# Kernel optimization log

Measured on AMD Instinct MI355X. Metric: run time of the kernel, lower is better.

Reference implementation:

```python
import jax, jax.numpy as jnp
import numpy as np
from jax import lax

K = 16        # patch_size / kernel_size
S = 16        # stride
EMB = 768     # embed_dim
CIN = 3


def setup_inputs() -> dict:
    key = jax.random.key(0)
    k1, k2, k3, k4, k5 = jax.random.split(key, 5)
    B, H, W = 64, 384, 384
    pixel_values = jax.random.normal(k1, (B, CIN, H, W), jnp.float32)
    # offset conv: Conv2d(3, 2*K*K, kernel=K, stride=K); small init so offsets stay moderate
    offset_w = jax.random.normal(k2, (2 * K * K, CIN, K, K), jnp.float32) * 0.01
    offset_b = jax.random.normal(k3, (2 * K * K,), jnp.float32) * 0.01
    # deformable projection: DeformConv2d(3, 768, kernel=K, stride=K)
    proj_w = jax.random.normal(k4, (EMB, CIN, K, K), jnp.float32) * 0.02
    proj_b = jax.random.normal(k5, (EMB,), jnp.float32) * 0.02
    return {"pixel_values": pixel_values, "offset_w": offset_w, "offset_b": offset_b,
            "proj_w": proj_w, "proj_b": proj_b}


def _bilinear_gather(img, py, px):
    """img: [B,C,H,W]; py,px: [B,K,K,HO,WO] float sample coords.
    Returns [B,C,K,K,HO,WO] with zero padding outside the image (torchvision semantics)."""
    B, C, H, W = img.shape
    shp = py.shape
    y0 = jnp.floor(py); x0 = jnp.floor(px)
    wy1 = py - y0; wy0 = 1.0 - wy1
    wx1 = px - x0; wx0 = 1.0 - wx1
    imgf = img.reshape(B, C, H * W)

    def corner(yy, xx, w):
        valid = (yy >= 0) & (yy < H) & (xx >= 0) & (xx < W)
        yi = jnp.clip(yy, 0, H - 1).astype(jnp.int32)
        xi = jnp.clip(xx, 0, W - 1).astype(jnp.int32)
        idx = (yi * W + xi).reshape(B, -1)                       # [B, N]
        v = jnp.take_along_axis(imgf, idx[:, None, :], axis=2)   # [B, C, N]
        return v * (jnp.where(valid, w, 0.0)).reshape(B, 1, -1)

    val = (corner(y0, x0, wy0 * wx0) + corner(y0, x0 + 1, wy0 * wx1)
           + corner(y0 + 1, x0, wy1 * wx0) + corner(y0 + 1, x0 + 1, wy1 * wx1))
    return val.reshape((B, C) + shp[1:])


def reference(pixel_values, offset_w, offset_b, proj_w, proj_b):
    B, C, H, W = pixel_values.shape
    HO, WO = H // S, W // S
    # offset conv (dense, stride=patch, VALID padding)
    offset = lax.conv_general_dilated(pixel_values, offset_w, (S, S), 'VALID',
                                      dimension_numbers=('NCHW', 'OIHW', 'NCHW'))
    offset = offset + offset_b[None, :, None, None]              # [B, 2*K*K, HO, WO]
    off = offset.reshape(B, K * K, 2, HO, WO)
    dy = off[:, :, 0].reshape(B, K, K, HO, WO)
    dx = off[:, :, 1].reshape(B, K, K, HO, WO)
    # base sampling grid: p = (ho*S + i + dy, wo*S + j + dx)
    base_y = (jnp.arange(HO, dtype=jnp.float32) * S)[None, None, None, :, None] \
             + jnp.arange(K, dtype=jnp.float32)[None, :, None, None, None]
    base_x = (jnp.arange(WO, dtype=jnp.float32) * S)[None, None, None, None, :] \
             + jnp.arange(K, dtype=jnp.float32)[None, None, :, None, None]
    py = base_y + dy
    px = base_x + dx
    sampled = _bilinear_gather(pixel_values, py, px)             # [B, C, K, K, HO, WO]
    out = jnp.einsum('bcijhw,ocij->bohw', sampled, proj_w) + proj_b[None, :, None, None]
    # flatten(2).transpose(1,2) -> [B, HO*WO, EMB]
    return out.reshape(B, EMB, HO * WO).transpose(0, 2, 1)
```

## Files before the change

kernel.cpp:

```cpp
#include <hip/hip_runtime.h>
#include <stdint.h>

typedef __bf16 bf16x8 __attribute__((ext_vector_type(8)));
typedef float  f32x4  __attribute__((ext_vector_type(4)));

#define HH 384
#define WW 384
#define NPIX (HH*WW)
#define NC 3
#define NPATCH 576
#define EMB 768
#define PLEN 768
#define MLOC 32
#define KSTEPS 24
#define NLOC (64*576)
#define NT1 4
#define NT2 6
#define W1_UNITS (32*KSTEPS*64)
#define W2_UNITS (48*KSTEPS*64)
#define W2_OFF   (W1_UNITS*8)

__device__ __forceinline__ uint16_t f2bf(float f) {
    uint32_t u = __builtin_bit_cast(uint32_t, f);
    u += 0x7FFFu + ((u >> 16) & 1u);
    return (uint16_t)(u >> 16);
}
__device__ __forceinline__ uint32_t pk2(float a, float b) {
    return (uint32_t)f2bf(a) | ((uint32_t)f2bf(b) << 16);
}

__global__ __launch_bounds__(256)
void convert_weights(const float* __restrict__ offw, const float* __restrict__ projw,
                     uint16_t* __restrict__ wz) {
    int u = blockIdx.x * 256 + threadIdx.x;
    const float* src;
    int uu;
    if (u < W1_UNITS) { src = offw; uu = u; }
    else              { src = projw; uu = u - W1_UNITS; }
    int lane = uu & 63;
    int t    = uu >> 6;
    int ks   = t % KSTEPS;
    int nt   = t / KSTEPS;
    int n    = nt * 16 + (lane & 15);
    int k0   = ks * 32 + (lane >> 4) * 8;
    const float4* s4 = (const float4*)(src + (size_t)n * PLEN + k0);
    float4 v0 = s4[0], v1 = s4[1];
    uint4 w;
    w.x = pk2(v0.x, v0.y); w.y = pk2(v0.z, v0.w);
    w.z = pk2(v1.x, v1.y); w.w = pk2(v1.z, v1.w);
    *(uint4*)(wz + (size_t)u * 8) = w;
}

template<bool USE_WS>
__global__ __launch_bounds__(512, 4)
void fused_kernel(const float* __restrict__ pix,
                  const float* __restrict__ offw,
                  const float* __restrict__ offb,
                  const float* __restrict__ projw,
                  const float* __restrict__ projb,
                  const uint16_t* __restrict__ wz,
                  float* __restrict__ out) {
    __shared__ __align__(16) uint16_t As[MLOC][PLEN];

    const int tid  = threadIdx.x;
    const int wv   = tid >> 6;
    const int lane = tid & 63;
    const int lr   = lane & 15;
    const int lg   = lane >> 4;

    int bid = (int)blockIdx.x;
    bid = (bid & 7) * 144 + (bid >> 3);

    const int loc0 = bid * MLOC;
    const int bimg = loc0 / NPATCH;
    const int p0   = loc0 - bimg * NPATCH;
    const float* __restrict__ pb = pix + (size_t)bimg * NC * NPIX;

    #pragma unroll
    for (int uu = 0; uu < 6; ++uu) {
        int unit = tid + uu * 512;
        int loc  = unit / 96;
        int k8   = (unit - loc * 96) * 8;
        int c  = k8 >> 8;
        int i  = (k8 >> 4) & 15;
        int j  = k8 & 15;
        int p  = p0 + loc;
        int ho = p / 24;
        int wo = p - ho * 24;
        const float* g = pb + ((size_t)c * HH + ho * 16 + i) * WW + wo * 16 + j;
        float4 v0 = *(const float4*)g;
        float4 v1 = *(const float4*)(g + 4);
        uint4 w;
        w.x = pk2(v0.x, v0.y); w.y = pk2(v0.z, v0.w);
        w.z = pk2(v1.x, v1.y); w.w = pk2(v1.z, v1.w);
        *(uint4*)&As[loc][k8 ^ ((loc & 7) << 3)] = w;
    }

    const int sw0 = (lr & 7) << 3;

    auto ldb1 = [&](int ntg, int ks) -> bf16x8 {
        if (USE_WS) {
            return *(const bf16x8*)(wz + ((size_t)((ntg * KSTEPS + ks) * 64 + lane)) * 8);
        } else {
            int n = ntg * 16 + lr;
            const float4* s4 = (const float4*)(offw + (size_t)n * PLEN + ks * 32 + lg * 8);
            float4 v0 = s4[0], v1 = s4[1];
            uint4 uq = {pk2(v0.x,v0.y), pk2(v0.z,v0.w), pk2(v1.x,v1.y), pk2(v1.z,v1.w)};
            return __builtin_bit_cast(bf16x8, uq);
        }
    };
    bf16x8 b1a[NT1], b1b[NT1];
    #pragma unroll
    for (int nt = 0; nt < NT1; ++nt) b1a[nt] = ldb1(wv * NT1 + nt, 0);
    __syncthreads();

    f32x4 acc1[2][NT1];
    #pragma unroll
    for (int nt = 0; nt < NT1; ++nt) {
        float bz = offb[(wv * NT1 + nt) * 16 + lr];
        f32x4 z = {bz, bz, bz, bz};
        acc1[0][nt] = z; acc1[1][nt] = z;
    }
    #pragma unroll 1
    for (int ks2 = 0; ks2 < KSTEPS / 2; ++ks2) {
        const int ks0 = ks2 * 2;
        {
            #pragma unroll
            for (int nt = 0; nt < NT1; ++nt) b1b[nt] = ldb1(wv * NT1 + nt, ks0 + 1);
            int ke = (ks0 * 32 + lg * 8) ^ sw0;
            bf16x8 a0 = *(const bf16x8*)&As[lr][ke];
            bf16x8 a1 = *(const bf16x8*)&As[16 + lr][ke];
            __builtin_amdgcn_s_setprio(1);
            #pragma unroll
            for (int nt = 0; nt < NT1; ++nt) {
                acc1[0][nt] = __builtin_amdgcn_mfma_f32_16x16x32_bf16(a0, b1a[nt], acc1[0][nt], 0, 0, 0);
                acc1[1][nt] = __builtin_amdgcn_mfma_f32_16x16x32_bf16(a1, b1a[nt], acc1[1][nt], 0, 0, 0);
            }
            __builtin_amdgcn_s_setprio(0);
        }
        {
            int ksn = (ks0 + 2 < KSTEPS) ? ks0 + 2 : 0;
            #pragma unroll
            for (int nt = 0; nt < NT1; ++nt) b1a[nt] = ldb1(wv * NT1 + nt, ksn);
            int ke = ((ks0 + 1) * 32 + lg * 8) ^ sw0;
            bf16x8 a0 = *(const bf16x8*)&As[lr][ke];
            bf16x8 a1 = *(const bf16x8*)&As[16 + lr][ke];
            __builtin_amdgcn_s_setprio(1);
            #pragma unroll
            for (int nt = 0; nt < NT1; ++nt) {
                acc1[0][nt] = __builtin_amdgcn_mfma_f32_16x16x32_bf16(a0, b1b[nt], acc1[0][nt], 0, 0, 0);
                acc1[1][nt] = __builtin_amdgcn_mfma_f32_16x16x32_bf16(a1, b1b[nt], acc1[1][nt], 0, 0, 0);
            }
            __builtin_amdgcn_s_setprio(0);
        }
    }
    __syncthreads();

    const int even = ((lane & 1) == 0);
    float dyg[2][2][4], dxg[2][2][4];
    #pragma unroll
    for (int nt = 0; nt < NT1; ++nt)
      #pragma unroll
      for (int mt = 0; mt < 2; ++mt)
        #pragma unroll
        for (int r = 0; r < 4; ++r) {
            float v  = acc1[mt][nt][r];
            float pv = __shfl_xor(v, 1);
            if ((nt < 2) == (even != 0)) {
                int s = nt & 1;
                dyg[s][mt][r] = even ? v  : pv;
                dxg[s][mt][r] = even ? pv : v;
            }
        }

    const int ntb  = wv * NT1 + (even ? 0 : 2);
    const int qlow = lr >> 1;
    #pragma unroll
    for (int s = 0; s < 2; ++s) {
        int q  = (ntb + s) * 8 + qlow;
        int qi = q >> 4;
        int qj = q & 15;
        #pragma unroll
        for (int mt = 0; mt < 2; ++mt)
          #pragma unroll
          for (int r = 0; r < 4; ++r) {
            int locl = mt * 16 + lg * 4 + r;
            int p  = p0 + locl;
            int ho = p / 24;
            int wo = p - ho * 24;
            float py = (float)(ho * 16 + qi) + dyg[s][mt][r];
            float px = (float)(wo * 16 + qj) + dxg[s][mt][r];
            float y0f = floorf(py), x0f = floorf(px);
            float wy1 = py - y0f, wy0 = 1.f - wy1;
            float wx1 = px - x0f, wx0 = 1.f - wx1;
            int y0 = (int)y0f, x0 = (int)x0f;
            float s0 = 0.f, s1 = 0.f, s2 = 0.f;
            #pragma unroll
            for (int cy = 0; cy < 2; ++cy) {
                int yy = y0 + cy;
                if ((unsigned)yy < (unsigned)HH) {
                    float wy = cy ? wy1 : wy0;
                    #pragma unroll
                    for (int cx = 0; cx < 2; ++cx) {
                        int xx = x0 + cx;
                        if ((unsigned)xx < (unsigned)WW) {
                            float w = wy * (cx ? wx1 : wx0);
                            const float* cp = pb + yy * WW + xx;
                            s0 += w * cp[0];
                            s1 += w * cp[NPIX];
                            s2 += w * cp[2 * NPIX];
                        }
                    }
                }
            }
            int swl = (locl & 7) << 3;
            As[locl][(      q) ^ swl] = f2bf(s0);
            As[locl][(256 + q) ^ swl] = f2bf(s1);
            As[locl][(512 + q) ^ swl] = f2bf(s2);
          }
    }

    auto ldb2 = [&](int ntg, int ks) -> bf16x8 {
        if (USE_WS) {
            return *(const bf16x8*)(wz + W2_OFF + ((size_t)((ntg * KSTEPS + ks) * 64 + lane)) * 8);
        } else {
            int n = ntg * 16 + lr;
            const float4* s4 = (const float4*)(projw + (size_t)n * PLEN + ks * 32 + lg * 8);
            float4 v0 = s4[0], v1 = s4[1];
            uint4 uq = {pk2(v0.x,v0.y), pk2(v0.z,v0.w), pk2(v1.x,v1.y), pk2(v1.z,v1.w)};
            return __builtin_bit_cast(bf16x8, uq);
        }
    };
    bf16x8 b2a[NT2], b2b[NT2];
    #pragma unroll
    for (int nt = 0; nt < NT2; ++nt) b2a[nt] = ldb2(wv * NT2 + nt, 0);
    __syncthreads();

    f32x4 acc2[2][NT2];
    #pragma unroll
    for (int nt = 0; nt < NT2; ++nt) {
        float bz = projb[(wv * NT2 + nt) * 16 + lr];
        f32x4 z = {bz, bz, bz, bz};
        acc2[0][nt] = z; acc2[1][nt] = z;
    }
    #pragma unroll 1
    for (int ks2 = 0; ks2 < KSTEPS / 2; ++ks2) {
        const int ks0 = ks2 * 2;
        {
            #pragma unroll
            for (int nt = 0; nt < NT2; ++nt) b2b[nt] = ldb2(wv * NT2 + nt, ks0 + 1);
            int ke = (ks0 * 32 + lg * 8) ^ sw0;
            bf16x8 a0 = *(const bf16x8*)&As[lr][ke];
            bf16x8 a1 = *(const bf16x8*)&As[16 + lr][ke];
            __builtin_amdgcn_s_setprio(1);
            #pragma unroll
            for (int nt = 0; nt < NT2; ++nt) {
                acc2[0][nt] = __builtin_amdgcn_mfma_f32_16x16x32_bf16(a0, b2a[nt], acc2[0][nt], 0, 0, 0);
                acc2[1][nt] = __builtin_amdgcn_mfma_f32_16x16x32_bf16(a1, b2a[nt], acc2[1][nt], 0, 0, 0);
            }
            __builtin_amdgcn_s_setprio(0);
        }
        {
            int ksn = (ks0 + 2 < KSTEPS) ? ks0 + 2 : 0;
            #pragma unroll
            for (int nt = 0; nt < NT2; ++nt) b2a[nt] = ldb2(wv * NT2 + nt, ksn);
            int ke = ((ks0 + 1) * 32 + lg * 8) ^ sw0;
            bf16x8 a0 = *(const bf16x8*)&As[lr][ke];
            bf16x8 a1 = *(const bf16x8*)&As[16 + lr][ke];
            __builtin_amdgcn_s_setprio(1);
            #pragma unroll
            for (int nt = 0; nt < NT2; ++nt) {
                acc2[0][nt] = __builtin_amdgcn_mfma_f32_16x16x32_bf16(a0, b2b[nt], acc2[0][nt], 0, 0, 0);
                acc2[1][nt] = __builtin_amdgcn_mfma_f32_16x16x32_bf16(a1, b2b[nt], acc2[1][nt], 0, 0, 0);
            }
            __builtin_amdgcn_s_setprio(0);
        }
    }

    #pragma unroll
    for (int mt = 0; mt < 2; ++mt)
      #pragma unroll
      for (int r = 0; r < 4; ++r) {
        int flat = loc0 + mt * 16 + lg * 4 + r;
        float* op = out + (size_t)flat * EMB;
        #pragma unroll
        for (int nt = 0; nt < NT2; ++nt)
            op[(wv * NT2 + nt) * 16 + lr] = acc2[mt][nt][r];
      }
}

extern "C" void kernel_launch(void* const* d_in, const int* in_sizes, int n_in,
                              void* d_out, int out_size, void* d_ws, size_t ws_size,
                              hipStream_t stream) {
    const float* pix   = (const float*)d_in[0];
    const float* offw  = (const float*)d_in[1];
    const float* offb  = (const float*)d_in[2];
    const float* projw = (const float*)d_in[3];
    const float* projb = (const float*)d_in[4];
    float* out = (float*)d_out;
    uint16_t* wz = (uint16_t*)d_ws;

    const size_t ws_needed = (size_t)(W1_UNITS + W2_UNITS) * 16;
    dim3 grid(NLOC / MLOC);

    if (ws_size >= ws_needed) {
        convert_weights<<<(W1_UNITS + W2_UNITS) / 256, 256, 0, stream>>>(offw, projw, wz);
        fused_kernel<true><<<grid, 512, 0, stream>>>(pix, offw, offb, projw, projb, wz, out);
    } else {
        fused_kernel<false><<<grid, 512, 0, stream>>>(pix, offw, offb, projw, projb, wz, out);
    }
}
```

Baseline: 206.3 us.

## Pre-pack pixels as interleaved bf16 and remap bilinear sampling through LDS offsets

A prepass now also converts the whole image into a channel-interleaved bf16 layout (4 halves per pixel), so each bilinear corner fetch is one 8-byte load instead of three strided fp32 loads. Offsets from the first GEMM are staged in LDS as packed bf16 pairs and the sampling loop is remapped so each wave handles whole patches with lanes covering consecutive kernel positions, improving gather locality. The cost is an extra full read and write pass over the image (about 113MB read, 75MB written), another 32KB of LDS per block that may reduce occupancy, and lower precision, since both the offsets and the sampled pixels are now rounded to bf16.

```diff
diff --git a/kernel.cpp b/kernel.cpp
--- a/kernel.cpp
+++ b/kernel.cpp
@@ -14,11 +14,16 @@
 #define MLOC 32
 #define KSTEPS 24
 #define NLOC (64*576)
+#define NTILES (NLOC/MLOC)
 #define NT1 4
 #define NT2 6
 #define W1_UNITS (32*KSTEPS*64)
 #define W2_UNITS (48*KSTEPS*64)
 #define W2_OFF   (W1_UNITS*8)
+#define PXP_OFF  ((W1_UNITS+W2_UNITS)*8)
+#define NPIX_TOT (64*NPIX)
+#define WBLKS  ((W1_UNITS + W2_UNITS) / 256)
+#define PXBLKS (NPIX_TOT / (256*4))
 
 __device__ __forceinline__ uint16_t f2bf(float f) {
     uint32_t u = __builtin_bit_cast(uint32_t, f);
@@ -28,27 +33,50 @@
 __device__ __forceinline__ uint32_t pk2(float a, float b) {
     return (uint32_t)f2bf(a) | ((uint32_t)f2bf(b) << 16);
 }
+__device__ __forceinline__ float bf2f(uint16_t u) {
+    return __builtin_bit_cast(float, (uint32_t)u << 16);
+}
 
 __global__ __launch_bounds__(256)
-void convert_weights(const float* __restrict__ offw, const float* __restrict__ projw,
-                     uint16_t* __restrict__ wz) {
-    int u = blockIdx.x * 256 + threadIdx.x;
-    const float* src;
-    int uu;
-    if (u < W1_UNITS) { src = offw; uu = u; }
-    else              { src = projw; uu = u - W1_UNITS; }
-    int lane = uu & 63;
-    int t    = uu >> 6;
-    int ks   = t % KSTEPS;
-    int nt   = t / KSTEPS;
-    int n    = nt * 16 + (lane & 15);
-    int k0   = ks * 32 + (lane >> 4) * 8;
-    const float4* s4 = (const float4*)(src + (size_t)n * PLEN + k0);
-    float4 v0 = s4[0], v1 = s4[1];
-    uint4 w;
-    w.x = pk2(v0.x, v0.y); w.y = pk2(v0.z, v0.w);
-    w.z = pk2(v1.x, v1.y); w.w = pk2(v1.z, v1.w);
-    *(uint4*)(wz + (size_t)u * 8) = w;
+void prepass(const float* __restrict__ offw, const float* __restrict__ projw,
+             const float* __restrict__ pix, uint16_t* __restrict__ wz) {
+    int b = blockIdx.x;
+    if (b < WBLKS) {
+        int u = b * 256 + threadIdx.x;
+        const float* src;
+        int uu;
+        if (u < W1_UNITS) { src = offw; uu = u; }
+        else              { src = projw; uu = u - W1_UNITS; }
+        int lane = uu & 63;
+        int t    = uu >> 6;
+        int ks   = t % KSTEPS;
+        int nt   = t / KSTEPS;
+        int n    = nt * 16 + (lane & 15);
+        int k0   = ks * 32 + (lane >> 4) * 8;
+        const float4* s4 = (const float4*)(src + (size_t)n * PLEN + k0);
+        float4 v0 = s4[0], v1 = s4[1];
+        uint4 w;
+        w.x = pk2(v0.x, v0.y); w.y = pk2(v0.z, v0.w);
+        w.z = pk2(v1.x, v1.y); w.w = pk2(v1.z, v1.w);
+        *(uint4*)(wz + (size_t)u * 8) = w;
+    } else {
+        int idx  = (b - WBLKS) * 256 + threadIdx.x;
+        int base = idx * 4;
+        int im = base / NPIX;
+        int yx = base - im * NPIX;
+        const float* p = pix + (size_t)im * NC * NPIX + yx;
+        float4 c0 = *(const float4*)p;
+        float4 c1 = *(const float4*)(p + NPIX);
+        float4 c2 = *(const float4*)(p + 2 * NPIX);
+        uint4 o0, o1;
+        o0.x = pk2(c0.x, c1.x); o0.y = (uint32_t)f2bf(c2.x);
+        o0.z = pk2(c0.y, c1.y); o0.w = (uint32_t)f2bf(c2.y);
+        o1.x = pk2(c0.z, c1.z); o1.y = (uint32_t)f2bf(c2.z);
+        o1.z = pk2(c0.w, c1.w); o1.w = (uint32_t)f2bf(c2.w);
+        uint16_t* dst = wz + PXP_OFF + (size_t)base * 4;
+        *(uint4*)dst       = o0;
+        *(uint4*)(dst + 8) = o1;
+    }
 }
 
 template<bool USE_WS>
@@ -61,20 +89,24 @@
                   const uint16_t* __restrict__ wz,
                   float* __restrict__ out) {
     __shared__ __align__(16) uint16_t As[MLOC][PLEN];
+    __shared__ uint32_t Offs[MLOC][256];
 
     const int tid  = threadIdx.x;
     const int wv   = tid >> 6;
     const int lane = tid & 63;
     const int lr   = lane & 15;
     const int lg   = lane >> 4;
+    const int sw0  = (lr & 7) << 3;
+    const int even = ((lane & 1) == 0);
 
     int bid = (int)blockIdx.x;
-    bid = (bid & 7) * 144 + (bid >> 3);
-
-    const int loc0 = bid * MLOC;
+    const int tile = (bid & 7) * 144 + (bid >> 3);
+
+    const int loc0 = tile * MLOC;
     const int bimg = loc0 / NPATCH;
     const int p0   = loc0 - bimg * NPATCH;
-    const float* __restrict__ pb = pix + (size_t)bimg * NC * NPIX;
+    const float*    __restrict__ pb  = pix + (size_t)bimg * NC * NPIX;
+    const uint16_t* __restrict__ pxp = wz + PXP_OFF + (size_t)bimg * NPIX * 4;
 
     #pragma unroll
     for (int uu = 0; uu < 6; ++uu) {
@@ -96,8 +128,6 @@
         *(uint4*)&As[loc][k8 ^ ((loc & 7) << 3)] = w;
     }
 
-    const int sw0 = (lr & 7) << 3;
-
     auto ldb1 = [&](int ntg, int ks) -> bf16x8 {
         if (USE_WS) {
             return *(const bf16x8*)(wz + ((size_t)((ntg * KSTEPS + ks) * 64 + lane)) * 8);
@@ -154,10 +184,7 @@
             __builtin_amdgcn_s_setprio(0);
         }
     }
-    __syncthreads();
-
-    const int even = ((lane & 1) == 0);
-    float dyg[2][2][4], dxg[2][2][4];
+
     #pragma unroll
     for (int nt = 0; nt < NT1; ++nt)
       #pragma unroll
@@ -167,57 +194,71 @@
             float v  = acc1[mt][nt][r];
             float pv = __shfl_xor(v, 1);
             if ((nt < 2) == (even != 0)) {
-                int s = nt & 1;
-                dyg[s][mt][r] = even ? v  : pv;
-                dxg[s][mt][r] = even ? pv : v;
-            }
-        }
-
-    const int ntb  = wv * NT1 + (even ? 0 : 2);
-    const int qlow = lr >> 1;
-    #pragma unroll
-    for (int s = 0; s < 2; ++s) {
-        int q  = (ntb + s) * 8 + qlow;
-        int qi = q >> 4;
-        int qj = q & 15;
+                int s   = nt & 1;
+                int loc = mt * 16 + lg * 4 + r;
+                int q   = (wv * NT1 + (even ? 0 : 2) + s) * 8 + (lr >> 1);
+                float dy = even ? v  : pv;
+                float dx = even ? pv : v;
+                Offs[loc][q] = pk2(dy, dx);
+            }
+        }
+    __syncthreads();
+
+    {
         #pragma unroll
-        for (int mt = 0; mt < 2; ++mt)
-          #pragma unroll
-          for (int r = 0; r < 4; ++r) {
-            int locl = mt * 16 + lg * 4 + r;
-            int p  = p0 + locl;
-            int ho = p / 24;
-            int wo = p - ho * 24;
-            float py = (float)(ho * 16 + qi) + dyg[s][mt][r];
-            float px = (float)(wo * 16 + qj) + dxg[s][mt][r];
-            float y0f = floorf(py), x0f = floorf(px);
-            float wy1 = py - y0f, wy0 = 1.f - wy1;
-            float wx1 = px - x0f, wx0 = 1.f - wx1;
-            int y0 = (int)y0f, x0 = (int)x0f;
-            float s0 = 0.f, s1 = 0.f, s2 = 0.f;
-            #pragma unroll
-            for (int cy = 0; cy < 2; ++cy) {
-                int yy = y0 + cy;
-                if ((unsigned)yy < (unsigned)HH) {
-                    float wy = cy ? wy1 : wy0;
-                    #pragma unroll
-                    for (int cx = 0; cx < 2; ++cx) {
-                        int xx = x0 + cx;
-                        if ((unsigned)xx < (unsigned)WW) {
-                            float w = wy * (cx ? wx1 : wx0);
-                            const float* cp = pb + yy * WW + xx;
-                            s0 += w * cp[0];
-                            s1 += w * cp[NPIX];
-                            s2 += w * cp[2 * NPIX];
+        for (int li = 0; li < 4; ++li) {
+            const int L  = wv * 4 + li;
+            const int p  = p0 + L;
+            const int ho = p / 24;
+            const int wo = p - ho * 24;
+            const int swl = (L & 7) << 3;
+            const int by = ho * 16;
+            const int bx = wo * 16;
+            #pragma unroll
+            for (int s4 = 0; s4 < 4; ++s4) {
+                const int q  = s4 * 64 + lane;
+                const int qi = q >> 4;
+                const int qj = q & 15;
+                uint32_t od = Offs[L][q];
+                float dy = bf2f((uint16_t)od);
+                float dx = bf2f((uint16_t)(od >> 16));
+                float py = (float)(by + qi) + dy;
+                float px = (float)(bx + qj) + dx;
+                float y0f = floorf(py), x0f = floorf(px);
+                float wy1 = py - y0f, wy0 = 1.f - wy1;
+                float wx1 = px - x0f, wx0 = 1.f - wx1;
+                int y0 = (int)y0f, x0 = (int)x0f;
+                float s0 = 0.f, s1 = 0.f, s2 = 0.f;
+                #pragma unroll
+                for (int cy = 0; cy < 2; ++cy) {
+                    int yy = y0 + cy;
+                    if ((unsigned)yy < (unsigned)HH) {
+                        float wy = cy ? wy1 : wy0;
+                        #pragma unroll
+                        for (int cx = 0; cx < 2; ++cx) {
+                            int xx = x0 + cx;
+                            if ((unsigned)xx < (unsigned)WW) {
+                                float w = wy * (cx ? wx1 : wx0);
+                                float v0, v1, v2;
+                                if (USE_WS) {
+                                    uint2 d = *(const uint2*)(pxp + ((size_t)yy * WW + xx) * 4);
+                                    v0 = bf2f((uint16_t)d.x);
+                                    v1 = bf2f((uint16_t)(d.x >> 16));
+                                    v2 = bf2f((uint16_t)d.y);
+                                } else {
+                                    const float* cp = pb + yy * WW + xx;
+                                    v0 = cp[0]; v1 = cp[NPIX]; v2 = cp[2 * NPIX];
+                                }
+                                s0 += w * v0; s1 += w * v1; s2 += w * v2;
+                            }
                         }
                     }
                 }
-            }
-            int swl = (locl & 7) << 3;
-            As[locl][(      q) ^ swl] = f2bf(s0);
-            As[locl][(256 + q) ^ swl] = f2bf(s1);
-            As[locl][(512 + q) ^ swl] = f2bf(s2);
-          }
+                As[L][(      q) ^ swl] = f2bf(s0);
+                As[L][(256 + q) ^ swl] = f2bf(s1);
+                As[L][(512 + q) ^ swl] = f2bf(s2);
+            }
+        }
     }
 
     auto ldb2 = [&](int ntg, int ks) -> bf16x8 {
@@ -300,13 +341,12 @@
     float* out = (float*)d_out;
     uint16_t* wz = (uint16_t*)d_ws;
 
-    const size_t ws_needed = (size_t)(W1_UNITS + W2_UNITS) * 16;
-    dim3 grid(NLOC / MLOC);
+    const size_t ws_needed = (size_t)(W1_UNITS + W2_UNITS) * 16 + (size_t)NPIX_TOT * 8;
 
     if (ws_size >= ws_needed) {
-        convert_weights<<<(W1_UNITS + W2_UNITS) / 256, 256, 0, stream>>>(offw, projw, wz);
-        fused_kernel<true><<<grid, 512, 0, stream>>>(pix, offw, offb, projw, projb, wz, out);
+        prepass<<<WBLKS + PXBLKS, 256, 0, stream>>>(offw, projw, pix, wz);
+        fused_kernel<true><<<NTILES, 512, 0, stream>>>(pix, offw, offb, projw, projb, wz, out);
     } else {
-        fused_kernel<false><<<grid, 512, 0, stream>>>(pix, offw, offb, projw, projb, wz, out);
-    }
-}
+        fused_kernel<false><<<NTILES, 512, 0, stream>>>(pix, offw, offb, projw, projb, wz, out);
+    }
+}
```

Measured after the change: 214.7 us. +4.1%, slower.

## Split fused deformable patch-embed into offset, gather, and tiled projection kernels

Applied to the files above, without the earlier changes.

Breaks the single fused kernel into three launches: an offset GEMM that writes bf16 (dy,dx) pairs to a workspace buffer, a gather kernel that overwrites those rows with bilinear samples, and a separate projection GEMM using 128x128 tiles with double-buffered LDS staging. The aim is more weight reuse per block in the large projection GEMM and lower register and LDS pressure in each stage. In exchange it adds a round trip through global memory for the 37k x 768 bf16 sampled matrix plus two extra launches. The fallback path is replaced with a simple fp32 SIMT kernel.

```diff
diff --git a/kernel.cpp b/kernel.cpp
--- a/kernel.cpp
+++ b/kernel.cpp
@@ -14,11 +14,13 @@
 #define MLOC 32
 #define KSTEPS 24
 #define NLOC (64*576)
+#define NTILES (NLOC/MLOC)
 #define NT1 4
-#define NT2 6
 #define W1_UNITS (32*KSTEPS*64)
 #define W2_UNITS (48*KSTEPS*64)
 #define W2_OFF   (W1_UNITS*8)
+#define SA_OFF   ((W1_UNITS+W2_UNITS)*8)
+#define WBLKS  ((W1_UNITS + W2_UNITS) / 256)
 
 __device__ __forceinline__ uint16_t f2bf(float f) {
     uint32_t u = __builtin_bit_cast(uint32_t, f);
@@ -28,10 +30,13 @@
 __device__ __forceinline__ uint32_t pk2(float a, float b) {
     return (uint32_t)f2bf(a) | ((uint32_t)f2bf(b) << 16);
 }
+__device__ __forceinline__ float bf2f(uint16_t u) {
+    return __builtin_bit_cast(float, (uint32_t)u << 16);
+}
 
 __global__ __launch_bounds__(256)
-void convert_weights(const float* __restrict__ offw, const float* __restrict__ projw,
-                     uint16_t* __restrict__ wz) {
+void prepass_w(const float* __restrict__ offw, const float* __restrict__ projw,
+               uint16_t* __restrict__ wz) {
     int u = blockIdx.x * 256 + threadIdx.x;
     const float* src;
     int uu;
@@ -51,15 +56,11 @@
     *(uint4*)(wz + (size_t)u * 8) = w;
 }
 
-template<bool USE_WS>
 __global__ __launch_bounds__(512, 4)
-void fused_kernel(const float* __restrict__ pix,
-                  const float* __restrict__ offw,
-                  const float* __restrict__ offb,
-                  const float* __restrict__ projw,
-                  const float* __restrict__ projb,
-                  const uint16_t* __restrict__ wz,
-                  float* __restrict__ out) {
+void k1_offsets(const float* __restrict__ pix,
+                const float* __restrict__ offb,
+                const uint16_t* __restrict__ wz,
+                uint16_t* __restrict__ sa) {
     __shared__ __align__(16) uint16_t As[MLOC][PLEN];
 
     const int tid  = threadIdx.x;
@@ -67,11 +68,12 @@
     const int lane = tid & 63;
     const int lr   = lane & 15;
     const int lg   = lane >> 4;
+    const int sw0  = (lr & 7) << 3;
+    const int even = ((lane & 1) == 0);
 
     int bid = (int)blockIdx.x;
-    bid = (bid & 7) * 144 + (bid >> 3);
-
-    const int loc0 = bid * MLOC;
+    const int tile = (bid & 7) * 144 + (bid >> 3);
+    const int loc0 = tile * MLOC;
     const int bimg = loc0 / NPATCH;
     const int p0   = loc0 - bimg * NPATCH;
     const float* __restrict__ pb = pix + (size_t)bimg * NC * NPIX;
@@ -96,18 +98,8 @@
         *(uint4*)&As[loc][k8 ^ ((loc & 7) << 3)] = w;
     }
 
-    const int sw0 = (lr & 7) << 3;
-
     auto ldb1 = [&](int ntg, int ks) -> bf16x8 {
-        if (USE_WS) {
-            return *(const bf16x8*)(wz + ((size_t)((ntg * KSTEPS + ks) * 64 + lane)) * 8);
-        } else {
-            int n = ntg * 16 + lr;
-            const float4* s4 = (const float4*)(offw + (size_t)n * PLEN + ks * 32 + lg * 8);
-            float4 v0 = s4[0], v1 = s4[1];
-            uint4 uq = {pk2(v0.x,v0.y), pk2(v0.z,v0.w), pk2(v1.x,v1.y), pk2(v1.z,v1.w)};
-            return __builtin_bit_cast(bf16x8, uq);
-        }
+        return *(const bf16x8*)(wz + ((size_t)((ntg * KSTEPS + ks) * 64 + lane)) * 8);
     };
     bf16x8 b1a[NT1], b1b[NT1];
     #pragma unroll
@@ -130,13 +122,11 @@
             int ke = (ks0 * 32 + lg * 8) ^ sw0;
             bf16x8 a0 = *(const bf16x8*)&As[lr][ke];
             bf16x8 a1 = *(const bf16x8*)&As[16 + lr][ke];
-            __builtin_amdgcn_s_setprio(1);
             #pragma unroll
             for (int nt = 0; nt < NT1; ++nt) {
                 acc1[0][nt] = __builtin_amdgcn_mfma_f32_16x16x32_bf16(a0, b1a[nt], acc1[0][nt], 0, 0, 0);
                 acc1[1][nt] = __builtin_amdgcn_mfma_f32_16x16x32_bf16(a1, b1a[nt], acc1[1][nt], 0, 0, 0);
             }
-            __builtin_amdgcn_s_setprio(0);
         }
         {
             int ksn = (ks0 + 2 < KSTEPS) ? ks0 + 2 : 0;
@@ -145,19 +135,14 @@
             int ke = ((ks0 + 1) * 32 + lg * 8) ^ sw0;
             bf16x8 a0 = *(const bf16x8*)&As[lr][ke];
             bf16x8 a1 = *(const bf16x8*)&As[16 + lr][ke];
-            __builtin_amdgcn_s_setprio(1);
             #pragma unroll
             for (int nt = 0; nt < NT1; ++nt) {
                 acc1[0][nt] = __builtin_amdgcn_mfma_f32_16x16x32_bf16(a0, b1b[nt], acc1[0][nt], 0, 0, 0);
                 acc1[1][nt] = __builtin_amdgcn_mfma_f32_16x16x32_bf16(a1, b1b[nt], acc1[1][nt], 0, 0, 0);
             }
-            __builtin_amdgcn_s_setprio(0);
-        }
-    }
-    __syncthreads();
-
-    const int even = ((lane & 1) == 0);
-    float dyg[2][2][4], dxg[2][2][4];
+        }
+    }
+
     #pragma unroll
     for (int nt = 0; nt < NT1; ++nt)
       #pragma unroll
@@ -167,29 +152,54 @@
             float v  = acc1[mt][nt][r];
             float pv = __shfl_xor(v, 1);
             if ((nt < 2) == (even != 0)) {
-                int s = nt & 1;
-                dyg[s][mt][r] = even ? v  : pv;
-                dxg[s][mt][r] = even ? pv : v;
-            }
-        }
-
-    const int ntb  = wv * NT1 + (even ? 0 : 2);
-    const int qlow = lr >> 1;
-    #pragma unroll
-    for (int s = 0; s < 2; ++s) {
-        int q  = (ntb + s) * 8 + qlow;
-        int qi = q >> 4;
-        int qj = q & 15;
-        #pragma unroll
-        for (int mt = 0; mt < 2; ++mt)
-          #pragma unroll
-          for (int r = 0; r < 4; ++r) {
-            int locl = mt * 16 + lg * 4 + r;
-            int p  = p0 + locl;
-            int ho = p / 24;
-            int wo = p - ho * 24;
-            float py = (float)(ho * 16 + qi) + dyg[s][mt][r];
-            float px = (float)(wo * 16 + qj) + dxg[s][mt][r];
+                int s   = nt & 1;
+                int loc = mt * 16 + lg * 4 + r;
+                int q   = (wv * NT1 + (even ? 0 : 2) + s) * 8 + (lr >> 1);
+                float dy = even ? v  : pv;
+                float dx = even ? pv : v;
+                ((uint32_t*)(sa + (size_t)(loc0 + loc) * PLEN))[q] = pk2(dy, dx);
+            }
+        }
+}
+
+__global__ __launch_bounds__(512)
+void k2_gather(const float* __restrict__ pix, uint16_t* __restrict__ sa) {
+    const int tid  = threadIdx.x;
+    const int wv   = tid >> 6;
+    const int lane = tid & 63;
+
+    int bid = (int)blockIdx.x;
+    const int tile = (bid & 7) * 144 + (bid >> 3);
+    const int loc0 = tile * MLOC;
+    const int bimg = loc0 / NPATCH;
+    const int p0   = loc0 - bimg * NPATCH;
+    const float* __restrict__ pb = pix + (size_t)bimg * NC * NPIX;
+
+    #pragma unroll
+    for (int li = 0; li < 4; ++li) {
+        const int L   = wv * 4 + li;
+        const int p   = p0 + L;
+        const int ho  = p / 24;
+        const int wo  = p - ho * 24;
+        const int by  = ho * 16;
+        const int bx  = wo * 16;
+        uint16_t* row = sa + (size_t)(loc0 + L) * PLEN;
+        const uint32_t* rowu = (const uint32_t*)row;
+        uint32_t od0 = rowu[       lane];
+        uint32_t od1 = rowu[ 64 +  lane];
+        uint32_t od2 = rowu[128 +  lane];
+        uint32_t od3 = rowu[192 +  lane];
+        asm volatile("s_waitcnt vmcnt(0)" ::: "memory");
+        #pragma unroll
+        for (int s4 = 0; s4 < 4; ++s4) {
+            const int q  = s4 * 64 + lane;
+            const int qi = q >> 4;
+            const int qj = q & 15;
+            uint32_t od = (s4 == 0) ? od0 : (s4 == 1) ? od1 : (s4 == 2) ? od2 : od3;
+            float dy = bf2f((uint16_t)od);
+            float dx = bf2f((uint16_t)(od >> 16));
+            float py = (float)(by + qi) + dy;
+            float px = (float)(bx + qj) + dx;
             float y0f = floorf(py), x0f = floorf(px);
             float wy1 = py - y0f, wy0 = 1.f - wy1;
             float wx1 = px - x0f, wx0 = 1.f - wx1;
@@ -213,80 +223,225 @@
                     }
                 }
             }
-            int swl = (locl & 7) << 3;
-            As[locl][(      q) ^ swl] = f2bf(s0);
-            As[locl][(256 + q) ^ swl] = f2bf(s1);
-            As[locl][(512 + q) ^ swl] = f2bf(s2);
-          }
-    }
-
-    auto ldb2 = [&](int ntg, int ks) -> bf16x8 {
-        if (USE_WS) {
-            return *(const bf16x8*)(wz + W2_OFF + ((size_t)((ntg * KSTEPS + ks) * 64 + lane)) * 8);
-        } else {
-            int n = ntg * 16 + lr;
-            const float4* s4 = (const float4*)(projw + (size_t)n * PLEN + ks * 32 + lg * 8);
-            float4 v0 = s4[0], v1 = s4[1];
-            uint4 uq = {pk2(v0.x,v0.y), pk2(v0.z,v0.w), pk2(v1.x,v1.y), pk2(v1.z,v1.w)};
-            return __builtin_bit_cast(bf16x8, uq);
-        }
+            row[      q] = f2bf(s0);
+            row[256 + q] = f2bf(s1);
+            row[512 + q] = f2bf(s2);
+        }
+    }
+}
+
+__global__ __launch_bounds__(256, 3)
+void k3_proj(const uint16_t* __restrict__ wz, const float* __restrict__ projb,
+             float* __restrict__ out) {
+    __shared__ __align__(16) uint16_t Asb[2][128][64];
+
+    const int tid  = threadIdx.x;
+    const int wv   = tid >> 6;
+    const int lane = tid & 63;
+    const int lr   = lane & 15;
+    const int lg   = lane >> 4;
+    const int wm   = wv >> 1;
+    const int wn   = wv & 1;
+
+    int bid = (int)blockIdx.x;
+    const int fin   = (bid & 7) * 216 + (bid >> 3);
+    const int mtile = fin / 6;
+    const int ncol  = fin - mtile * 6;
+    const int loc0  = mtile * 128;
+    const int n0    = ncol * 128;
+    const uint16_t* __restrict__ sa = wz + SA_OFF;
+
+    const int srow = tid >> 1;
+    const int shalf = tid & 1;
+    const int srb = srow & 7;
+    const uint16_t* sg = sa + (size_t)(loc0 + srow) * PLEN + shalf * 32;
+
+    uint4 r0, r1, r2, r3;
+    auto st_load = [&](int t) {
+        const uint16_t* g = sg + t * 64;
+        r0 = *(const uint4*)g;
+        r1 = *(const uint4*)(g + 8);
+        r2 = *(const uint4*)(g + 16);
+        r3 = *(const uint4*)(g + 24);
     };
-    bf16x8 b2a[NT2], b2b[NT2];
-    #pragma unroll
-    for (int nt = 0; nt < NT2; ++nt) b2a[nt] = ldb2(wv * NT2 + nt, 0);
+    auto st_write = [&](int buf) {
+        uint16_t* dst = &Asb[buf][srow][0];
+        *(uint4*)(dst + (((shalf * 4 + 0) ^ srb) * 8)) = r0;
+        *(uint4*)(dst + (((shalf * 4 + 1) ^ srb) * 8)) = r1;
+        *(uint4*)(dst + (((shalf * 4 + 2) ^ srb) * 8)) = r2;
+        *(uint4*)(dst + (((shalf * 4 + 3) ^ srb) * 8)) = r3;
+    };
+    auto ldb = [&](int nt, int ks) -> bf16x8 {
+        int ntg = ncol * 8 + wn * 4 + nt;
+        return *(const bf16x8*)(wz + W2_OFF + ((size_t)((ntg * KSTEPS + ks) * 64 + lane)) * 8);
+    };
+
+    f32x4 acc[4][4];
+    #pragma unroll
+    for (int nt = 0; nt < 4; ++nt) {
+        float bz = projb[n0 + wn * 64 + nt * 16 + lr];
+        f32x4 z = {bz, bz, bz, bz};
+        #pragma unroll
+        for (int mi = 0; mi < 4; ++mi) acc[mi][nt] = z;
+    }
+
+    bf16x8 ba[4], bb[4];
+    st_load(0);
+    st_write(0);
+    #pragma unroll
+    for (int nt = 0; nt < 4; ++nt) ba[nt] = ldb(nt, 0);
     __syncthreads();
 
-    f32x4 acc2[2][NT2];
-    #pragma unroll
-    for (int nt = 0; nt < NT2; ++nt) {
-        float bz = projb[(wv * NT2 + nt) * 16 + lr];
-        f32x4 z = {bz, bz, bz, bz};
-        acc2[0][nt] = z; acc2[1][nt] = z;
-    }
     #pragma unroll 1
-    for (int ks2 = 0; ks2 < KSTEPS / 2; ++ks2) {
-        const int ks0 = ks2 * 2;
+    for (int t = 0; t < 12; ++t) {
+        const int cur = t & 1;
+        if (t < 11) st_load(t + 1);
         {
             #pragma unroll
-            for (int nt = 0; nt < NT2; ++nt) b2b[nt] = ldb2(wv * NT2 + nt, ks0 + 1);
-            int ke = (ks0 * 32 + lg * 8) ^ sw0;
-            bf16x8 a0 = *(const bf16x8*)&As[lr][ke];
-            bf16x8 a1 = *(const bf16x8*)&As[16 + lr][ke];
-            __builtin_amdgcn_s_setprio(1);
-            #pragma unroll
-            for (int nt = 0; nt < NT2; ++nt) {
-                acc2[0][nt] = __builtin_amdgcn_mfma_f32_16x16x32_bf16(a0, b2a[nt], acc2[0][nt], 0, 0, 0);
-                acc2[1][nt] = __builtin_amdgcn_mfma_f32_16x16x32_bf16(a1, b2a[nt], acc2[1][nt], 0, 0, 0);
-            }
-            __builtin_amdgcn_s_setprio(0);
+            for (int nt = 0; nt < 4; ++nt) bb[nt] = ldb(nt, t * 2 + 1);
+            bf16x8 a0, a1, a2, a3;
+            {
+                const int u = ((0 * 4 + lg) ^ (lr & 7)) * 8;
+                a0 = *(const bf16x8*)&Asb[cur][wm * 64 +  0 + lr][u];
+                a1 = *(const bf16x8*)&Asb[cur][wm * 64 + 16 + lr][u];
+                a2 = *(const bf16x8*)&Asb[cur][wm * 64 + 32 + lr][u];
+                a3 = *(const bf16x8*)&Asb[cur][wm * 64 + 48 + lr][u];
+            }
+            #pragma unroll
+            for (int nt = 0; nt < 4; ++nt) {
+                acc[0][nt] = __builtin_amdgcn_mfma_f32_16x16x32_bf16(a0, ba[nt], acc[0][nt], 0, 0, 0);
+                acc[1][nt] = __builtin_amdgcn_mfma_f32_16x16x32_bf16(a1, ba[nt], acc[1][nt], 0, 0, 0);
+                acc[2][nt] = __builtin_amdgcn_mfma_f32_16x16x32_bf16(a2, ba[nt], acc[2][nt], 0, 0, 0);
+                acc[3][nt] = __builtin_amdgcn_mfma_f32_16x16x32_bf16(a3, ba[nt], acc[3][nt], 0, 0, 0);
+            }
         }
         {
-            int ksn = (ks0 + 2 < KSTEPS) ? ks0 + 2 : 0;
-            #pragma unroll
-            for (int nt = 0; nt < NT2; ++nt) b2a[nt] = ldb2(wv * NT2 + nt, ksn);
-            int ke = ((ks0 + 1) * 32 + lg * 8) ^ sw0;
-            bf16x8 a0 = *(const bf16x8*)&As[lr][ke];
-            bf16x8 a1 = *(const bf16x8*)&As[16 + lr][ke];
-            __builtin_amdgcn_s_setprio(1);
-            #pragma unroll
-            for (int nt = 0; nt < NT2; ++nt) {
-                acc2[0][nt] = __builtin_amdgcn_mfma_f32_16x16x32_bf16(a0, b2b[nt], acc2[0][nt], 0, 0, 0);
-                acc2[1][nt] = __builtin_amdgcn_mfma_f32_16x16x32_bf16(a1, b2b[nt], acc2[1][nt], 0, 0, 0);
-            }
-            __builtin_amdgcn_s_setprio(0);
-        }
-    }
-
-    #pragma unroll
-    for (int mt = 0; mt < 2; ++mt)
+            if (t < 11) {
+                #pragma unroll
+                for (int nt = 0; nt < 4; ++nt) ba[nt] = ldb(nt, t * 2 + 2);
+            }
+            bf16x8 a0, a1, a2, a3;
+            {
+                const int u = ((1 * 4 + lg) ^ (lr & 7)) * 8;
+                a0 = *(const bf16x8*)&Asb[cur][wm * 64 +  0 + lr][u];
+                a1 = *(const bf16x8*)&Asb[cur][wm * 64 + 16 + lr][u];
+                a2 = *(const bf16x8*)&Asb[cur][wm * 64 + 32 + lr][u];
+                a3 = *(const bf16x8*)&Asb[cur][wm * 64 + 48 + lr][u];
+            }
+            #pragma unroll
+            for (int nt = 0; nt < 4; ++nt) {
+                acc[0][nt] = __builtin_amdgcn_mfma_f32_16x16x32_bf16(a0, bb[nt], acc[0][nt], 0, 0, 0);
+                acc[1][nt] = __builtin_amdgcn_mfma_f32_16x16x32_bf16(a1, bb[nt], acc[1][nt], 0, 0, 0);
+                acc[2][nt] = __builtin_amdgcn_mfma_f32_16x16x32_bf16(a2, bb[nt], acc[2][nt], 0, 0, 0);
+                acc[3][nt] = __builtin_amdgcn_mfma_f32_16x16x32_bf16(a3, bb[nt], acc[3][nt], 0, 0, 0);
+            }
+        }
+        if (t < 11) st_write(cur ^ 1);
+        __syncthreads();
+    }
+
+    #pragma unroll
+    for (int mi = 0; mi < 4; ++mi)
       #pragma unroll
       for (int r = 0; r < 4; ++r) {
-        int flat = loc0 + mt * 16 + lg * 4 + r;
-        float* op = out + (size_t)flat * EMB;
-        #pragma unroll
-        for (int nt = 0; nt < NT2; ++nt)
-            op[(wv * NT2 + nt) * 16 + lr] = acc2[mt][nt][r];
+        int rowg = loc0 + wm * 64 + mi * 16 + lg * 4 + r;
+        float* op = out + (size_t)rowg * EMB + n0 + wn * 64;
+        #pragma unroll
+        for (int nt = 0; nt < 4; ++nt)
+            op[nt * 16 + lr] = acc[mi][nt][r];
       }
+}
+
+__global__ __launch_bounds__(256)
+void fallback_kernel(const float* __restrict__ pix, const float* __restrict__ offw,
+                     const float* __restrict__ offb, const float* __restrict__ projw,
+                     const float* __restrict__ projb, float* __restrict__ out) {
+    __shared__ float buf[8][PLEN];
+    const int tid = threadIdx.x;
+    const int loc0 = blockIdx.x * 8;
+    #pragma unroll
+    for (int r = 0; r < 6; ++r) {
+        int item = tid + r * 256;
+        int l = item / 192, k = (item - l * 192) * 4;
+        int c = k >> 8, i = (k >> 4) & 15, j = k & 15;
+        int flat = loc0 + l, b = flat / NPATCH, p = flat - b * NPATCH;
+        int ho = p / 24, wo = p - ho * 24;
+        *(float4*)(&buf[l][k]) = *(const float4*)(pix +
+            (((size_t)b * NC + c) * HH + (size_t)ho * 16 + i) * WW + wo * 16 + j);
+    }
+    __syncthreads();
+    float dy[8], dx[8];
+    {
+        float a0[8], a1[8];
+        float b0 = offb[2 * tid], b1 = offb[2 * tid + 1];
+        #pragma unroll
+        for (int l = 0; l < 8; ++l) { a0[l] = b0; a1[l] = b1; }
+        const float4* w0 = (const float4*)(offw + (size_t)(2 * tid) * PLEN);
+        const float4* w1 = w0 + PLEN / 4;
+        for (int k4 = 0; k4 < PLEN / 4; ++k4) {
+            float4 wa = w0[k4], wb = w1[k4];
+            #pragma unroll
+            for (int l = 0; l < 8; ++l) {
+                float4 pv = *(const float4*)(&buf[l][k4 * 4]);
+                a0[l] += wa.x*pv.x + wa.y*pv.y + wa.z*pv.z + wa.w*pv.w;
+                a1[l] += wb.x*pv.x + wb.y*pv.y + wb.z*pv.z + wb.w*pv.w;
+            }
+        }
+        #pragma unroll
+        for (int l = 0; l < 8; ++l) { dy[l] = a0[l]; dx[l] = a1[l]; }
+    }
+    __syncthreads();
+    {
+        const int i = tid >> 4, j = tid & 15;
+        #pragma unroll
+        for (int l = 0; l < 8; ++l) {
+            int flat = loc0 + l, b = flat / NPATCH, p = flat - b * NPATCH;
+            int ho = p / 24, wo = p - ho * 24;
+            float py = (float)(ho * 16 + i) + dy[l];
+            float px = (float)(wo * 16 + j) + dx[l];
+            float y0 = floorf(py), x0 = floorf(px);
+            float wy1 = py - y0, wy0 = 1.f - wy1, wx1 = px - x0, wx0 = 1.f - wx1;
+            const float* pb = pix + (size_t)b * NC * NPIX;
+            float s0 = 0, s1 = 0, s2 = 0;
+            #pragma unroll
+            for (int cy = 0; cy < 2; ++cy)
+              #pragma unroll
+              for (int cx = 0; cx < 2; ++cx) {
+                int yy = (int)y0 + cy, xx = (int)x0 + cx;
+                float w = (cy ? wy1 : wy0) * (cx ? wx1 : wx0);
+                if ((unsigned)yy < (unsigned)HH && (unsigned)xx < (unsigned)WW) {
+                    int idx = yy * WW + xx;
+                    s0 += w * pb[idx]; s1 += w * pb[NPIX + idx]; s2 += w * pb[2*NPIX + idx];
+                }
+              }
+            buf[l][tid] = s0; buf[l][256 + tid] = s1; buf[l][512 + tid] = s2;
+        }
+    }
+    __syncthreads();
+    {
+        float aA[8], aB[8], aC[8];
+        float bA = projb[tid], bB = projb[tid + 256], bC = projb[tid + 512];
+        #pragma unroll
+        for (int l = 0; l < 8; ++l) { aA[l] = bA; aB[l] = bB; aC[l] = bC; }
+        const float4* wA = (const float4*)(projw + (size_t)tid * PLEN);
+        const float4* wB = (const float4*)(projw + (size_t)(tid + 256) * PLEN);
+        const float4* wC = (const float4*)(projw + (size_t)(tid + 512) * PLEN);
+        for (int k4 = 0; k4 < PLEN / 4; ++k4) {
+            float4 a = wA[k4], bq = wB[k4], cq = wC[k4];
+            #pragma unroll
+            for (int l = 0; l < 8; ++l) {
+                float4 pv = *(const float4*)(&buf[l][k4 * 4]);
+                aA[l] += a.x*pv.x + a.y*pv.y + a.z*pv.z + a.w*pv.w;
+                aB[l] += bq.x*pv.x + bq.y*pv.y + bq.z*pv.z + bq.w*pv.w;
+                aC[l] += cq.x*pv.x + cq.y*pv.y + cq.z*pv.z + cq.w*pv.w;
+            }
+        }
+        #pragma unroll
+        for (int l = 0; l < 8; ++l) {
+            float* op = out + (size_t)(loc0 + l) * EMB;
+            op[tid] = aA[l]; op[tid + 256] = aB[l]; op[tid + 512] = aC[l];
+        }
+    }
 }
 
 extern "C" void kernel_launch(void* const* d_in, const int* in_sizes, int n_in,
@@ -300,13 +455,15 @@
     float* out = (float*)d_out;
     uint16_t* wz = (uint16_t*)d_ws;
 
-    const size_t ws_needed = (size_t)(W1_UNITS + W2_UNITS) * 16;
-    dim3 grid(NLOC / MLOC);
+    const size_t ws_needed = (size_t)SA_OFF * 2 + (size_t)NLOC * PLEN * 2;
 
     if (ws_size >= ws_needed) {
-        convert_weights<<<(W1_UNITS + W2_UNITS) / 256, 256, 0, stream>>>(offw, projw, wz);
-        fused_kernel<true><<<grid, 512, 0, stream>>>(pix, offw, offb, projw, projb, wz, out);
+        uint16_t* sa = wz + SA_OFF;
+        prepass_w<<<WBLKS, 256, 0, stream>>>(offw, projw, wz);
+        k1_offsets<<<NTILES, 512, 0, stream>>>(pix, offb, wz, sa);
+        k2_gather<<<NTILES, 512, 0, stream>>>(pix, sa);
+        k3_proj<<<288 * 6, 256, 0, stream>>>(wz, projb, out);
     } else {
-        fused_kernel<false><<<grid, 512, 0, stream>>>(pix, offw, offb, projw, projb, wz, out);
-    }
-}
+        fallback_kernel<<<NLOC / 8, 256, 0, stream>>>(pix, offw, offb, projw, projb, out);
+    }
+}
```

Result: slower. 215.6 us (+4.5%).
